# Performance work log

Measured on AMD Instinct MI355X. Metric: run time of the kernel, lower is better.

## Reference

```python
import jax, jax.numpy as jnp
import numpy as np

B, S, E = 4, 2048, 1024


def setup_inputs() -> dict:
    key = jax.random.key(0)
    ks = jax.random.split(key, 7)
    sc = 1.0 / np.sqrt(E)
    return {
        "embedded": jax.random.normal(ks[0], (B, S, E), dtype=jnp.float32),
        "Wk": jax.random.normal(ks[1], (E, E), dtype=jnp.float32) * sc,
        "bk": jax.random.normal(ks[2], (E,), dtype=jnp.float32) * 0.01,
        "Wq": jax.random.normal(ks[3], (E, E), dtype=jnp.float32) * sc,
        "bq": jax.random.normal(ks[4], (E,), dtype=jnp.float32) * 0.01,
        "Wv": jax.random.normal(ks[5], (E, E), dtype=jnp.float32) * sc,
        "bv": jax.random.normal(ks[6], (E,), dtype=jnp.float32) * 0.01,
    }


def reference(embedded, Wk, bk, Wq, bq, Wv, bv):
    # embedded: [B, S, E]
    K = embedded @ Wk.T + bk  # [B,S,E]
    Q = embedded @ Wq.T + bq
    V = embedded @ Wv.T + bv
    seq_len = K.shape[1]
    # score[b,i,j] = K_i . Q_j, scaled by 1/sqrt(seq_len) (as in original)
    scores = jnp.einsum('bie,bje->bij', K, Q) / jnp.sqrt(jnp.asarray(seq_len, K.dtype))
    # softmax over dim=-2 -> over the key index i
    W = jax.nn.softmax(scores, axis=-2)  # [B,S,S]
    # Y = (V^T @ W)^T -> Y[b,j,d] = sum_i V[b,i,d] * W[b,i,j]
    Y = jnp.einsum('bid,bij->bjd', V, W)  # [B,S,E]
    return Y
```

## Files before the change

### kernel.cpp

```cpp
#include <hip/hip_runtime.h>
#include <hip/hip_bf16.h>


typedef __bf16 bf16x8 __attribute__((ext_vector_type(8)));
typedef float  f32x4  __attribute__((ext_vector_type(4)));

__device__ __forceinline__ unsigned short f2bf(float f) {
    unsigned int u = __float_as_uint(f);
    u = (u + 0x7FFFu + ((u >> 16) & 1u)) >> 16;
    return (unsigned short)u;
}

__global__ __launch_bounds__(256)
void cvt_all(const float* __restrict__ X,  const float* __restrict__ Wq,
             const float* __restrict__ Wk, const float* __restrict__ Wv,
             unsigned short* __restrict__ Xb,  unsigned short* __restrict__ Wqb,
             unsigned short* __restrict__ Wkb, unsigned short* __restrict__ Wvb,
             float* __restrict__ l) {
    long i = (long)blockIdx.x * 256 + threadIdx.x;
    if (i < 8192) l[i] = 0.0f;
    const float* src; unsigned short* dst; long off;
    if (i < 2097152L) { src = X; dst = Xb; off = i; }
    else {
        long j = i - 2097152L;
        int w = (int)(j >> 18);
        off = j & 262143L;
        src = (w == 0) ? Wq : (w == 1) ? Wk : Wv;
        dst = (w == 0) ? Wqb : (w == 1) ? Wkb : Wvb;
    }
    float4 v = reinterpret_cast<const float4*>(src)[off];
    ushort4 o;
    o.x = f2bf(v.x); o.y = f2bf(v.y); o.z = f2bf(v.z); o.w = f2bf(v.w);
    reinterpret_cast<ushort4*>(dst)[off] = o;
}

#define GEMM_DECLS                                                      \
    const int t    = threadIdx.x;                                       \
    const int wave = t >> 6;                                            \
    const int lane = t & 63;                                            \
    const int quad = lane >> 4;                                         \
    const int lr   = lane & 15;                                         \
    const int wm   = (wave >> 1) * 64;                                  \
    const int wn   = (wave & 1) * 64;                                   \
    const int sx   = lr & 7;                                            \
    const int lrow = lane >> 3;                                         \
    const int gch  = ((lane & 7) ^ (lrow & 7)) * 8;

#define GEMM_KLOOP(Aptr, Bptr, LDA, LDB)                                \
    for (int k0 = 0; k0 < K; k0 += 64) {                                \
        _Pragma("unroll")                                               \
        for (int r = 0; r < 4; ++r) {                                   \
            const int rowb = wave * 8 + r * 32;                         \
            const int row  = rowb + lrow;                               \
            const long goffA = (long)(m0 + row) * (LDA) + k0 + gch;     \
            const long goffB = (long)(n0 + row) * (LDB) + k0 + gch;     \
            __builtin_amdgcn_global_load_lds(                           \
                (const __attribute__((address_space(1))) void*)((Aptr) + goffA), \
                (__attribute__((address_space(3))) void*)(&lsA[rowb * 64]), 16, 0, 0); \
            __builtin_amdgcn_global_load_lds(                           \
                (const __attribute__((address_space(1))) void*)((Bptr) + goffB), \
                (__attribute__((address_space(3))) void*)(&lsB[rowb * 64]), 16, 0, 0); \
        }                                                               \
        __syncthreads();                                                \
        _Pragma("unroll")                                               \
        for (int h = 0; h < 2; ++h) {                                   \
            const int cp = ((h * 4 + quad) ^ sx) * 8;                   \
            bf16x8 af[4], bfr[4];                                       \
            _Pragma("unroll")                                           \
            for (int i = 0; i < 4; ++i) {                               \
                af[i]  = __builtin_bit_cast(bf16x8,                     \
                          *reinterpret_cast<const uint4*>(&lsA[(wm + i * 16 + lr) * 64 + cp])); \
                bfr[i] = __builtin_bit_cast(bf16x8,                     \
                          *reinterpret_cast<const uint4*>(&lsB[(wn + i * 16 + lr) * 64 + cp])); \
            }                                                           \
            _Pragma("unroll")                                           \
            for (int i = 0; i < 4; ++i)                                 \
                _Pragma("unroll")                                       \
                for (int j = 0; j < 4; ++j)                             \
                    acc[i][j] = __builtin_amdgcn_mfma_f32_16x16x32_bf16(af[i], bfr[j], acc[i][j], 0, 0, 0); \
        }                                                               \
        __syncthreads();                                                \
    }

__global__ __launch_bounds__(256, 2)
void gemm_qkv(const unsigned short* __restrict__ Xb,
              const unsigned short* __restrict__ Wqb,
              const unsigned short* __restrict__ Wkb,
              const unsigned short* __restrict__ Wvb,
              const float* __restrict__ bq, const float* __restrict__ bk,
              const float* __restrict__ bv_,
              unsigned short* __restrict__ Qb, unsigned short* __restrict__ Kb,
              unsigned short* __restrict__ Vt)
{
    __shared__ unsigned short lsA[128 * 64];
    __shared__ unsigned short lsB[128 * 64];

    const int id  = blockIdx.x;
    const int g   = id & 7;
    const int jj  = id >> 3;
    const int xx  = jj & 7;
    const int yin = (jj >> 3) & 7;
    const int z   = jj >> 6;

    const unsigned short* A = Xb;
    const unsigned short* B = (z == 0) ? Wqb : (z == 1) ? Wkb : Wvb;
    const float* bias       = (z == 0) ? bq  : (z == 1) ? bk  : bv_;

    const int n0 = xx * 128;
    const int m0 = (g * 8 + yin) * 128;
    const int K = 1024;

    GEMM_DECLS
    f32x4 acc[4][4] = {};
    GEMM_KLOOP(A, B, 1024, 1024)

#pragma unroll
    for (int j = 0; j < 4; ++j) {
        const int n = n0 + wn + j * 16 + lr;
        const float bvv = bias[n];
#pragma unroll
        for (int i = 0; i < 4; ++i) {
            const int mbase = m0 + wm + i * 16 + quad * 4;
            if (z < 2) {
                unsigned short* C = (z == 0) ? Qb : Kb;
#pragma unroll
                for (int r = 0; r < 4; ++r)
                    C[(long)(mbase + r) * 1024 + n] = f2bf(acc[i][j][r] + bvv);
            } else {
                ushort4 o;
                o.x = f2bf(acc[i][j][0] + bvv);
                o.y = f2bf(acc[i][j][1] + bvv);
                o.z = f2bf(acc[i][j][2] + bvv);
                o.w = f2bf(acc[i][j][3] + bvv);
                long boff = (long)(mbase >> 11) * (1024L * 2048) + (long)n * 2048 + (mbase & 2047);
                *reinterpret_cast<ushort4*>(Vt + boff) = o;
            }
        }
    }
}


#define VMW(N) asm volatile("s_waitcnt vmcnt(" #N ")" ::: "memory")

#define PIPE_DECLS                                                          \
    const int tid  = threadIdx.x;                                           \
    const int wave = tid >> 6;                                              \
    const int lane = tid & 63;                                              \
    const int quad = lane >> 4;                                             \
    const int lr   = lane & 15;                                             \
    const int wvm  = wave >> 2;                           \
    const int wvn  = wave & 3;                            \
    const int rd_off = (lr >> 1) * 64 + (lr & 1) * 32                       \
                     + ((quad ^ ((lr >> 1) & 3)) << 3);                     \
    const int stg_rl = wave * 16 + ((lane >> 3) << 1) + ((lane >> 2) & 1);  \
    const int stg_c  = (((lane & 3) ^ ((lane >> 3) & 3)) << 3);

#define ST1(base, LD, kcol, dst, c)                                         \
    __builtin_amdgcn_global_load_lds(                                       \
        (const __attribute__((address_space(1))) void*)                     \
            ((base) + (long)(c) * 128 * (LD) + (kcol)),                     \
        (__attribute__((address_space(3))) void*)(&lds[(dst) + (c) * 4096 + wave * 512]), \
        16, 0, 0)

#define PHASE(bs, h, mh, IH_, STG, WAITS)                                   \
    {                                                                       \
        if ((mh) == 0) {                                                    \
            _Pragma("unroll")                                               \
            for (int j = 0; j < 4; ++j)                                     \
                bfr[j] = __builtin_bit_cast(bf16x8,                         \
                    *reinterpret_cast<const uint4*>(                        \
                        &lds[BOFF(bs, h) + (wvn * 4 + j) * 512 + rd_off])); \
        }                                                                   \
        bf16x8 af[IH_];                                                     \
        _Pragma("unroll")                                                   \
        for (int i = 0; i < (IH_); ++i)                                     \
            af[i] = __builtin_bit_cast(bf16x8,                              \
                *reinterpret_cast<const uint4*>(                            \
                    &lds[AOFF(bs, h) + (wvm * 2 * (IH_) + (mh) * (IH_) + i) * 512 + rd_off])); \
        STG;                                                                \
        WAITS;                                                              \
        __builtin_amdgcn_s_barrier();                                       \
        __builtin_amdgcn_s_setprio(1);                                      \
        _Pragma("unroll")                                                   \
        for (int i = 0; i < (IH_); ++i)                                     \
            _Pragma("unroll")                                               \
            for (int j = 0; j < 4; ++j)                                     \
                acc[(mh) * (IH_) + i][j] = __builtin_amdgcn_mfma_f32_16x16x32_bf16( \
                    af[i], bfr[j], acc[(mh) * (IH_) + i][j], 0, 0, 0);      \
        __builtin_amdgcn_s_setprio(0);                                      \
        __builtin_amdgcn_s_barrier();                                       \
    }

#define RUN_PIPELINE(IH_, NT_, WAITST)                                      \
    f32x4 acc[2 * (IH_)][4] = {};                                           \
    bf16x8 bfr[4];                                                          \
    SA(0, 0, 0); SB(0, 0, 0); SA(0, 1, 0); SB(0, 1, 0); SA(1, 0, 1); SB(1, 0, 1); \
    WAITST;                                                                 \
    __builtin_amdgcn_s_barrier();                                           \
    _Pragma("unroll 1")                                                     \
    for (int it = 0; it < (NT_) / 2 - 1; ++it) {                            \
        const int tb = 2 * it;                                              \
        PHASE(0, 0, 0, IH_, SA(tb + 1, 1, 1), )                             \
        PHASE(0, 0, 1, IH_, SB(tb + 1, 1, 1), )                             \
        PHASE(0, 1, 0, IH_, SA(tb + 2, 0, 0), )                             \
        PHASE(0, 1, 1, IH_, SB(tb + 2, 0, 0), WAITST)                       \
        PHASE(1, 0, 0, IH_, SA(tb + 2, 1, 0), )                             \
        PHASE(1, 0, 1, IH_, SB(tb + 2, 1, 0), )                             \
        PHASE(1, 1, 0, IH_, SA(tb + 3, 0, 1), )                             \
        PHASE(1, 1, 1, IH_, SB(tb + 3, 0, 1), WAITST)                       \
    }                                                                       \
    PHASE(0, 0, 0, IH_, SA((NT_) - 1, 1, 1), )                              \
    PHASE(0, 0, 1, IH_, SB((NT_) - 1, 1, 1), )                              \
    PHASE(0, 1, 0, IH_, , )                                                 \
    PHASE(0, 1, 1, IH_, , WAITST)                                           \
    PHASE(1, 0, 0, IH_, , )                                                 \
    PHASE(1, 0, 1, IH_, , VMW(0))                                           \
    PHASE(1, 1, 0, IH_, , )                                                 \
    PHASE(1, 1, 1, IH_, , )

#define AOFF(b, h) ((b) * 32768 + (h) * 8192)
#define BOFF(b, h) ((b) * 32768 + 16384 + (h) * 8192)
#define SA(tt, h, b) { ST1(aBase, 1024, (tt) * 64 + (h) * 32, AOFF(b, h), 0); \
                       ST1(aBase, 1024, (tt) * 64 + (h) * 32, AOFF(b, h), 1); }
#define SB(tt, h, b) { ST1(bBase, 1024, (tt) * 64 + (h) * 32, BOFF(b, h), 0); \
                       ST1(bBase, 1024, (tt) * 64 + (h) * 32, BOFF(b, h), 1); }

__global__ __launch_bounds__(512, 2)
void gemm_scores(const unsigned short* __restrict__ Q,
                 const unsigned short* __restrict__ Kp,
                 unsigned short* __restrict__ P, float* __restrict__ l,
                 float scale)
{
    __shared__ __align__(16) unsigned short lds[65536];

    const int id = blockIdx.x;
    const int g  = id & 7;
    const int u  = id >> 3;
    const int bz = g >> 1;
    const int m0 = ((g & 1) * 4 + (u & 3)) * 256;
    const int n0 = (u >> 2) * 256;

    const unsigned short* Aptr = Q  + (long)bz * 2048 * 1024;
    const unsigned short* Bptr = Kp + (long)bz * 2048 * 1024;
    unsigned short* Pb = P + (long)bz * 2048 * 2048;
    float* lb = l + bz * 2048;

    PIPE_DECLS
    const unsigned short* aBase = Aptr + (long)(m0 + stg_rl) * 1024 + stg_c;
    const unsigned short* bBase = Bptr + (long)(n0 + stg_rl) * 1024 + stg_c;

    RUN_PIPELINE(4, 16, VMW(4))

#pragma unroll
    for (int i = 0; i < 8; ++i) {
#pragma unroll
        for (int r = 0; r < 4; ++r) {
            const int m = m0 + wvm * 128 + i * 16 + quad * 4 + r;
            float psum = 0.0f;
#pragma unroll
            for (int j = 0; j < 4; ++j) {
                const float p = __expf(acc[i][j][r] * scale);
                psum += p;
                Pb[(long)m * 2048 + (n0 + wvn * 64 + j * 16 + lr)] = f2bf(p);
            }
#pragma unroll
            for (int o = 1; o < 16; o <<= 1) psum += __shfl_xor(psum, o, 64);
            if (lr == 0) atomicAdd(&lb[m], psum);
        }
    }
}

#undef SA
#undef SB
#undef AOFF
#undef BOFF

#define AOFF(b, h) ((b) * 24576 + (h) * 4096)
#define BOFF(b, h) ((b) * 24576 + 8192 + (h) * 8192)
#define SA(tt, h, b) { ST1(aBase, 2048, (tt) * 64 + (h) * 32, AOFF(b, h), 0); }
#define SB(tt, h, b) { ST1(bBase, 2048, (tt) * 64 + (h) * 32, BOFF(b, h), 0); \
                       ST1(bBase, 2048, (tt) * 64 + (h) * 32, BOFF(b, h), 1); }

__global__ __launch_bounds__(512, 2)
void gemm_y(const unsigned short* __restrict__ P,
            const unsigned short* __restrict__ Vt,
            const float* __restrict__ l, float* __restrict__ out)
{
    __shared__ __align__(16) unsigned short lds[49152];

    const int id = blockIdx.x;
    const int g  = id & 7;
    const int u  = id >> 3;
    const int bz = g >> 1;
    const int m0 = ((g & 1) * 8 + (u & 7)) * 128;
    const int n0 = (u >> 3) * 256;

    const unsigned short* Aptr = P  + (long)bz * 2048 * 2048;
    const unsigned short* Bptr = Vt + (long)bz * 1024 * 2048;
    const float* lb = l + bz * 2048;
    float* C = out + (long)bz * 2048 * 1024;

    PIPE_DECLS
    const unsigned short* aBase = Aptr + (long)(m0 + stg_rl) * 2048 + stg_c;
    const unsigned short* bBase = Bptr + (long)(n0 + stg_rl) * 2048 + stg_c;

    RUN_PIPELINE(2, 32, VMW(3))

    float linv[4][4];
#pragma unroll
    for (int i = 0; i < 4; ++i)
#pragma unroll
        for (int r = 0; r < 4; ++r)
            linv[i][r] = 1.0f / lb[m0 + wvm * 64 + i * 16 + quad * 4 + r];

#pragma unroll
    for (int j = 0; j < 4; ++j) {
        const int n = n0 + wvn * 64 + j * 16 + lr;
#pragma unroll
        for (int i = 0; i < 4; ++i) {
            const int mbase = m0 + wvm * 64 + i * 16 + quad * 4;
#pragma unroll
            for (int r = 0; r < 4; ++r)
                C[(long)(mbase + r) * 1024 + n] = acc[i][j][r] * linv[i][r];
        }
    }
}

#undef SA
#undef SB
#undef AOFF
#undef BOFF

extern "C" void kernel_launch(void* const* d_in, const int* in_sizes, int n_in,
                              void* d_out, int out_size, void* d_ws, size_t ws_size,
                              hipStream_t stream) {
    const float* X  = (const float*)d_in[0];
    const float* Wk = (const float*)d_in[1];
    const float* bk = (const float*)d_in[2];
    const float* Wq = (const float*)d_in[3];
    const float* bq = (const float*)d_in[4];
    const float* Wv = (const float*)d_in[5];
    const float* bv = (const float*)d_in[6];
    float* out = (float*)d_out;

    const size_t MB = 1024 * 1024;
    if (ws_size < 80 * MB) return;

    char* ws = (char*)d_ws;
    unsigned short* Vt  = (unsigned short*)(ws);
    unsigned short* P   = (unsigned short*)(ws + 16 * MB);
    unsigned short* Xbf = (unsigned short*)(ws + 16 * MB);
    float*          l   = (float*)(ws + 48 * MB);
    unsigned short* Wqb = (unsigned short*)(ws + 49 * MB);
    unsigned short* Wkb = (unsigned short*)(ws + 51 * MB);
    unsigned short* Wvb = (unsigned short*)(ws + 53 * MB);
    unsigned short* Qb = (unsigned short*)d_out;
    unsigned short* Kb = Qb + 8192L * 1024;

    cvt_all<<<2883584 / 256, dim3(256), 0, stream>>>(X, Wq, Wk, Wv, Xbf, Wqb, Wkb, Wvb, l);

    gemm_qkv<<<1536, dim3(256), 0, stream>>>(Xbf, Wqb, Wkb, Wvb, bq, bk, bv, Qb, Kb, Vt);

    gemm_scores<<<256, dim3(512), 0, stream>>>(Qb, Kb, P, l, 0.022097086912079608f);

    gemm_y<<<256, dim3(512), 0, stream>>>(P, Vt, l, out);
}
```

Measured before the change: 228.5 us.

## Retile gemm_y to 256x128 with a 4-buffer, 3-deep K-32 LDS pipeline

The P·V GEMM block tile changes from 128x256 to 256x128 (M x N), and the shared pipeline macro is replaced by a custom 4-stage ring of 32-wide K slices with three loads in flight. Each phase reads fragments from LDS, issues the next global-to-LDS copies, waits, then runs 16 MFMAs at raised priority. The aim is more latency hiding for global loads and a better balance between loading A (P) and B (V). The cost is more barriers per unit of K and different LDS traffic per MFMA.

```diff
diff --git a/kernel.cpp b/kernel.cpp
--- a/kernel.cpp
+++ b/kernel.cpp
@@ -275,11 +275,38 @@
 #undef AOFF
 #undef BOFF
 
-#define AOFF(b, h) ((b) * 24576 + (h) * 4096)
-#define BOFF(b, h) ((b) * 24576 + 8192 + (h) * 8192)
-#define SA(tt, h, b) { ST1(aBase, 2048, (tt) * 64 + (h) * 32, AOFF(b, h), 0); }
-#define SB(tt, h, b) { ST1(bBase, 2048, (tt) * 64 + (h) * 32, BOFF(b, h), 0); \
-                       ST1(bBase, 2048, (tt) * 64 + (h) * 32, BOFF(b, h), 1); }
+#define YAOFF(b) ((b) * 12288)
+#define YBOFF(b) ((b) * 12288 + 8192)
+#define YSA(tt, b) { ST1(aBase, 2048, (tt) * 32, YAOFF(b), 0); \
+                     ST1(aBase, 2048, (tt) * 32, YAOFF(b), 1); }
+#define YSB(tt, b) { ST1(bBase, 2048, (tt) * 32, YBOFF(b), 0); }
+
+#define YPHASE(bb, STG, WAITS)                                              \
+    {                                                                       \
+        bf16x8 af[4], bfr[4];                                               \
+        _Pragma("unroll")                                                   \
+        for (int j = 0; j < 4; ++j)                                         \
+            bfr[j] = __builtin_bit_cast(bf16x8,                             \
+                *reinterpret_cast<const uint4*>(                            \
+                    &lds[YBOFF(bb) + (wvn * 4 + j) * 512 + rd_off]));       \
+        _Pragma("unroll")                                                   \
+        for (int i = 0; i < 4; ++i)                                         \
+            af[i] = __builtin_bit_cast(bf16x8,                              \
+                *reinterpret_cast<const uint4*>(                            \
+                    &lds[YAOFF(bb) + (wvm * 4 + i) * 512 + rd_off]));       \
+        STG;                                                                \
+        WAITS;                                                              \
+        __builtin_amdgcn_s_barrier();                                       \
+        __builtin_amdgcn_s_setprio(1);                                      \
+        _Pragma("unroll")                                                   \
+        for (int i = 0; i < 4; ++i)                                         \
+            _Pragma("unroll")                                               \
+            for (int j = 0; j < 4; ++j)                                     \
+                acc[i][j] = __builtin_amdgcn_mfma_f32_16x16x32_bf16(        \
+                    af[i], bfr[j], acc[i][j], 0, 0, 0);                     \
+        __builtin_amdgcn_s_setprio(0);                                      \
+        __builtin_amdgcn_s_barrier();                                       \
+    }
 
 __global__ __launch_bounds__(512, 2)
 void gemm_y(const unsigned short* __restrict__ P,
@@ -292,19 +319,47 @@
     const int g  = id & 7;
     const int u  = id >> 3;
     const int bz = g >> 1;
-    const int m0 = ((g & 1) * 8 + (u & 7)) * 128;
-    const int n0 = (u >> 3) * 256;
+    const int m0 = ((g & 1) * 4 + (u & 3)) * 256;
+    const int n0 = (u >> 2) * 128;
 
     const unsigned short* Aptr = P  + (long)bz * 2048 * 2048;
     const unsigned short* Bptr = Vt + (long)bz * 1024 * 2048;
     const float* lb = l + bz * 2048;
     float* C = out + (long)bz * 2048 * 1024;
 
-    PIPE_DECLS
+    const int tid  = threadIdx.x;
+    const int wave = tid >> 6;
+    const int lane = tid & 63;
+    const int quad = lane >> 4;
+    const int lr   = lane & 15;
+    const int wvm  = wave >> 1;
+    const int wvn  = wave & 1;
+    const int rd_off = (lr >> 1) * 64 + (lr & 1) * 32
+                     + ((quad ^ ((lr >> 1) & 3)) << 3);
+    const int stg_rl = wave * 16 + ((lane >> 3) << 1) + ((lane >> 2) & 1);
+    const int stg_c  = (((lane & 3) ^ ((lane >> 3) & 3)) << 3);
+
     const unsigned short* aBase = Aptr + (long)(m0 + stg_rl) * 2048 + stg_c;
     const unsigned short* bBase = Bptr + (long)(n0 + stg_rl) * 2048 + stg_c;
 
-    RUN_PIPELINE(2, 32, VMW(3))
+    f32x4 acc[4][4] = {};
+
+    YSA(0, 0); YSB(0, 0);
+    YSA(1, 1); YSB(1, 1);
+    YSA(2, 2); YSB(2, 2);
+    VMW(6);
+    __builtin_amdgcn_s_barrier();
+
+    int bcur = 0;
+#pragma unroll 1
+    for (int tt = 0; tt < 61; ++tt) {
+        int b3 = bcur + 3; if (b3 >= 4) b3 -= 4;
+        YPHASE(bcur, { YSA(tt + 3, b3); YSB(tt + 3, b3); }, VMW(6))
+        if (++bcur == 4) bcur = 0;
+    }
+    YPHASE(1, , VMW(3))
+    YPHASE(2, , VMW(0))
+    YPHASE(3, , )
 
     float linv[4][4];
 #pragma unroll
@@ -326,10 +381,10 @@
     }
 }
 
-#undef SA
-#undef SB
-#undef AOFF
-#undef BOFF
+#undef YSA
+#undef YSB
+#undef YAOFF
+#undef YBOFF
 
 extern "C" void kernel_launch(void* const* d_in, const int* in_sizes, int n_in,
                               void* d_out, int out_size, void* d_ws, size_t ws_size,
```

Result: slower. 240.9 us (+5.4%).

## Replace pipelined scores GEMM with simpler 128x256-tile kernel at higher occupancy

Applied to the files above, without the earlier changes.

The scores GEMM moves from the deep software-pipelined 256x256 tile kernel with 512 threads to a simple single-buffered 128x256 tile kernel with 256 threads and 3 blocks per CU, launched as 512 blocks. Each k-step loads A and B into LDS via global_load_lds, synchronises, and runs MFMAs. The aim is more resident blocks and fewer idle CUs instead of hand-tuned intra-block overlap. In exchange it drops the explicit load/compute pipelining, has a barrier after every tile, and gives more B-tile reloads per unit of output because the tiles are smaller.

```diff
diff --git a/kernel.cpp b/kernel.cpp
--- a/kernel.cpp
+++ b/kernel.cpp
@@ -139,6 +139,97 @@
     }
 }
 
+__global__ __launch_bounds__(256, 3)
+void gemm_scores(const unsigned short* __restrict__ Q,
+                 const unsigned short* __restrict__ Kp,
+                 unsigned short* __restrict__ P, float* __restrict__ l,
+                 float scale)
+{
+    __shared__ unsigned short lsA[128 * 64];
+    __shared__ unsigned short lsB[256 * 64];
+
+    const int id = blockIdx.x;
+    const int g  = id & 7;
+    const int u  = id >> 3;
+    const int bz = g >> 1;
+    const int m0 = ((g & 1) * 8 + (u & 7)) * 128;
+    const int n0 = (u >> 3) * 256;
+
+    const unsigned short* A = Q  + (long)bz * 2048 * 1024;
+    const unsigned short* B = Kp + (long)bz * 2048 * 1024;
+    unsigned short* Pb = P + (long)bz * 2048 * 2048;
+    float* lb = l + bz * 2048;
+
+    const int t    = threadIdx.x;
+    const int wave = t >> 6;
+    const int lane = t & 63;
+    const int quad = lane >> 4;
+    const int lr   = lane & 15;
+    const int sx   = lr & 7;
+    const int lrow = lane >> 3;
+    const int gch  = ((lane & 7) ^ (lrow & 7)) * 8;
+
+    f32x4 acc[8][4] = {};
+
+    for (int k0 = 0; k0 < 1024; k0 += 64) {
+#pragma unroll
+        for (int r = 0; r < 4; ++r) {
+            const int rowb = wave * 8 + r * 32;
+            __builtin_amdgcn_global_load_lds(
+                (const __attribute__((address_space(1))) void*)
+                    (A + (long)(m0 + rowb + lrow) * 1024 + k0 + gch),
+                (__attribute__((address_space(3))) void*)(&lsA[rowb * 64]), 16, 0, 0);
+        }
+#pragma unroll
+        for (int r = 0; r < 8; ++r) {
+            const int rowb = wave * 8 + r * 32;
+            __builtin_amdgcn_global_load_lds(
+                (const __attribute__((address_space(1))) void*)
+                    (B + (long)(n0 + rowb + lrow) * 1024 + k0 + gch),
+                (__attribute__((address_space(3))) void*)(&lsB[rowb * 64]), 16, 0, 0);
+        }
+        __syncthreads();
+#pragma unroll
+        for (int h = 0; h < 2; ++h) {
+            const int cp = ((h * 4 + quad) ^ sx) * 8;
+            bf16x8 af[8], bfr[4];
+#pragma unroll
+            for (int i = 0; i < 8; ++i)
+                af[i] = __builtin_bit_cast(bf16x8,
+                    *reinterpret_cast<const uint4*>(&lsA[(i * 16 + lr) * 64 + cp]));
+#pragma unroll
+            for (int j = 0; j < 4; ++j)
+                bfr[j] = __builtin_bit_cast(bf16x8,
+                    *reinterpret_cast<const uint4*>(&lsB[(wave * 64 + j * 16 + lr) * 64 + cp]));
+#pragma unroll
+            for (int i = 0; i < 8; ++i)
+#pragma unroll
+                for (int j = 0; j < 4; ++j)
+                    acc[i][j] = __builtin_amdgcn_mfma_f32_16x16x32_bf16(
+                        af[i], bfr[j], acc[i][j], 0, 0, 0);
+        }
+        __syncthreads();
+    }
+
+#pragma unroll
+    for (int i = 0; i < 8; ++i) {
+#pragma unroll
+        for (int r = 0; r < 4; ++r) {
+            const int m = m0 + i * 16 + quad * 4 + r;
+            float psum = 0.0f;
+#pragma unroll
+            for (int j = 0; j < 4; ++j) {
+                const float p = __expf(acc[i][j][r] * scale);
+                psum += p;
+                Pb[(long)m * 2048 + (n0 + wave * 64 + j * 16 + lr)] = f2bf(p);
+            }
+#pragma unroll
+            for (int o = 1; o < 16; o <<= 1) psum += __shfl_xor(psum, o, 64);
+            if (lr == 0) atomicAdd(&lb[m], psum);
+        }
+    }
+}
+
 
 #define VMW(N) asm volatile("s_waitcnt vmcnt(" #N ")" ::: "memory")
 
@@ -218,63 +309,6 @@
     PHASE(1, 1, 0, IH_, , )                                                 \
     PHASE(1, 1, 1, IH_, , )
 
-#define AOFF(b, h) ((b) * 32768 + (h) * 8192)
-#define BOFF(b, h) ((b) * 32768 + 16384 + (h) * 8192)
-#define SA(tt, h, b) { ST1(aBase, 1024, (tt) * 64 + (h) * 32, AOFF(b, h), 0); \
-                       ST1(aBase, 1024, (tt) * 64 + (h) * 32, AOFF(b, h), 1); }
-#define SB(tt, h, b) { ST1(bBase, 1024, (tt) * 64 + (h) * 32, BOFF(b, h), 0); \
-                       ST1(bBase, 1024, (tt) * 64 + (h) * 32, BOFF(b, h), 1); }
-
-__global__ __launch_bounds__(512, 2)
-void gemm_scores(const unsigned short* __restrict__ Q,
-                 const unsigned short* __restrict__ Kp,
-                 unsigned short* __restrict__ P, float* __restrict__ l,
-                 float scale)
-{
-    __shared__ __align__(16) unsigned short lds[65536];
-
-    const int id = blockIdx.x;
-    const int g  = id & 7;
-    const int u  = id >> 3;
-    const int bz = g >> 1;
-    const int m0 = ((g & 1) * 4 + (u & 3)) * 256;
-    const int n0 = (u >> 2) * 256;
-
-    const unsigned short* Aptr = Q  + (long)bz * 2048 * 1024;
-    const unsigned short* Bptr = Kp + (long)bz * 2048 * 1024;
-    unsigned short* Pb = P + (long)bz * 2048 * 2048;
-    float* lb = l + bz * 2048;
-
-    PIPE_DECLS
-    const unsigned short* aBase = Aptr + (long)(m0 + stg_rl) * 1024 + stg_c;
-    const unsigned short* bBase = Bptr + (long)(n0 + stg_rl) * 1024 + stg_c;
-
-    RUN_PIPELINE(4, 16, VMW(4))
-
-#pragma unroll
-    for (int i = 0; i < 8; ++i) {
-#pragma unroll
-        for (int r = 0; r < 4; ++r) {
-            const int m = m0 + wvm * 128 + i * 16 + quad * 4 + r;
-            float psum = 0.0f;
-#pragma unroll
-            for (int j = 0; j < 4; ++j) {
-                const float p = __expf(acc[i][j][r] * scale);
-                psum += p;
-                Pb[(long)m * 2048 + (n0 + wvn * 64 + j * 16 + lr)] = f2bf(p);
-            }
-#pragma unroll
-            for (int o = 1; o < 16; o <<= 1) psum += __shfl_xor(psum, o, 64);
-            if (lr == 0) atomicAdd(&lb[m], psum);
-        }
-    }
-}
-
-#undef SA
-#undef SB
-#undef AOFF
-#undef BOFF
-
 #define AOFF(b, h) ((b) * 24576 + (h) * 4096)
 #define BOFF(b, h) ((b) * 24576 + 8192 + (h) * 8192)
 #define SA(tt, h, b) { ST1(aBase, 2048, (tt) * 64 + (h) * 32, AOFF(b, h), 0); }
@@ -361,7 +395,7 @@
 
     gemm_qkv<<<1536, dim3(256), 0, stream>>>(Xbf, Wqb, Wkb, Wvb, bq, bk, bv, Qb, Kb, Vt);
 
-    gemm_scores<<<256, dim3(512), 0, stream>>>(Qb, Kb, P, l, 0.022097086912079608f);
+    gemm_scores<<<512, dim3(256), 0, stream>>>(Qb, Kb, P, l, 0.022097086912079608f);
 
     gemm_y<<<256, dim3(512), 0, stream>>>(P, Vt, l, out);
 }
```

Measured after the change: 256.6 us. 12.3% more time.

## Fold key/query projections into single X·(WkᵀWq) product and drop softmax-invariant bias terms

Applied to the files above, without the earlier changes.

Rewrites the score computation algebraically. It precomputes M = Wq^T Wk, projects X once through M instead of computing Q and K separately, and adds a per-key bias term u = X·(Wk^T bq). Terms depending only on the query index are dropped because they cancel in the softmax over keys. This removes one of the three large projection GEMMs at the cost of a small weight-weight GEMM, transposes and matvecs, and it adds an extra bf16 rounding of M.

```diff
diff --git a/kernel.cpp b/kernel.cpp
--- a/kernel.cpp
+++ b/kernel.cpp
@@ -10,28 +10,55 @@
     u = (u + 0x7FFFu + ((u >> 16) & 1u)) >> 16;
     return (unsigned short)u;
 }
+__device__ __forceinline__ float bf2f(unsigned short s) {
+    return __uint_as_float(((unsigned int)s) << 16);
+}
 
 __global__ __launch_bounds__(256)
 void cvt_all(const float* __restrict__ X,  const float* __restrict__ Wq,
              const float* __restrict__ Wk, const float* __restrict__ Wv,
-             unsigned short* __restrict__ Xb,  unsigned short* __restrict__ Wqb,
-             unsigned short* __restrict__ Wkb, unsigned short* __restrict__ Wvb,
+             unsigned short* __restrict__ Xb,  unsigned short* __restrict__ WqT,
+             unsigned short* __restrict__ WkT, unsigned short* __restrict__ Wvb,
              float* __restrict__ l) {
-    long i = (long)blockIdx.x * 256 + threadIdx.x;
-    if (i < 8192) l[i] = 0.0f;
-    const float* src; unsigned short* dst; long off;
-    if (i < 2097152L) { src = X; dst = Xb; off = i; }
-    else {
-        long j = i - 2097152L;
-        int w = (int)(j >> 18);
-        off = j & 262143L;
-        src = (w == 0) ? Wq : (w == 1) ? Wk : Wv;
-        dst = (w == 0) ? Wqb : (w == 1) ? Wkb : Wvb;
-    }
-    float4 v = reinterpret_cast<const float4*>(src)[off];
-    ushort4 o;
-    o.x = f2bf(v.x); o.y = f2bf(v.y); o.z = f2bf(v.z); o.w = f2bf(v.w);
-    reinterpret_cast<ushort4*>(dst)[off] = o;
+    __shared__ unsigned short lt[64][68];
+    const int id = blockIdx.x;
+    const int t  = threadIdx.x;
+    if (id < 9216) {
+        long i; const float* src; unsigned short* dst;
+        if (id < 8192) { i = (long)id * 256 + t; if (i < 8192) l[i] = 0.0f; src = X; dst = Xb; }
+        else           { i = (long)(id - 8192) * 256 + t; src = Wv; dst = Wvb; }
+        float4 v = reinterpret_cast<const float4*>(src)[i];
+        ushort4 o;
+        o.x = f2bf(v.x); o.y = f2bf(v.y); o.z = f2bf(v.z); o.w = f2bf(v.w);
+        reinterpret_cast<ushort4*>(dst)[i] = o;
+        return;
+    }
+    const int k   = id - 9216;
+    const int mat = k >> 8;
+    const int tl  = k & 255;
+    const int f0  = (tl >> 4) * 64;
+    const int e0  = (tl & 15) * 64;
+    const float* src = (mat == 0) ? Wq : Wk;
+    unsigned short* dst = (mat == 0) ? WqT : WkT;
+    const int r  = t >> 4;
+    const int c  = t & 15;
+#pragma unroll
+    for (int q = 0; q < 4; ++q) {
+        const int fl = r + q * 16;
+        float4 v = reinterpret_cast<const float4*>(src)[(long)(f0 + fl) * 256 + (e0 >> 2) + c];
+        lt[fl][c * 4 + 0] = f2bf(v.x); lt[fl][c * 4 + 1] = f2bf(v.y);
+        lt[fl][c * 4 + 2] = f2bf(v.z); lt[fl][c * 4 + 3] = f2bf(v.w);
+    }
+    __syncthreads();
+#pragma unroll
+    for (int q = 0; q < 4; ++q) {
+        const int el = (t >> 4) + q * 16;
+        const int f4 = (t & 15) * 4;
+        ushort4 o;
+        o.x = lt[f4 + 0][el]; o.y = lt[f4 + 1][el];
+        o.z = lt[f4 + 2][el]; o.w = lt[f4 + 3][el];
+        *reinterpret_cast<ushort4*>(&dst[(long)(e0 + el) * 1024 + f0 + f4]) = o;
+    }
 }
 
 #define GEMM_DECLS                                                      \
@@ -83,19 +110,92 @@
     }
 
 __global__ __launch_bounds__(256, 2)
-void gemm_qkv(const unsigned short* __restrict__ Xb,
-              const unsigned short* __restrict__ Wqb,
-              const unsigned short* __restrict__ Wkb,
-              const unsigned short* __restrict__ Wvb,
-              const float* __restrict__ bq, const float* __restrict__ bk,
-              const float* __restrict__ bv_,
-              unsigned short* __restrict__ Qb, unsigned short* __restrict__ Kb,
-              unsigned short* __restrict__ Vt)
+void prep(const unsigned short* __restrict__ WqT,
+          const unsigned short* __restrict__ WkT,
+          const float* __restrict__ bq,
+          unsigned short* __restrict__ Mt, float* __restrict__ w)
 {
     __shared__ unsigned short lsA[128 * 64];
     __shared__ unsigned short lsB[128 * 64];
-
-    const int id  = blockIdx.x;
+    const int id = blockIdx.x;
+    if (id < 64) {
+        const int m0 = (id & 7) * 128;
+        const int n0 = (id >> 3) * 128;
+        const int K = 1024;
+        GEMM_DECLS
+        f32x4 acc[4][4] = {};
+        GEMM_KLOOP(WqT, WkT, 1024, 1024)
+#pragma unroll
+        for (int j = 0; j < 4; ++j) {
+            const int n = n0 + wn + j * 16 + lr;
+#pragma unroll
+            for (int i = 0; i < 4; ++i) {
+                const int mbase = m0 + wm + i * 16 + quad * 4;
+#pragma unroll
+                for (int r = 0; r < 4; ++r)
+                    Mt[(long)(mbase + r) * 1024 + n] = f2bf(acc[i][j][r]);
+            }
+        }
+        return;
+    }
+    const int t2   = threadIdx.x;
+    const int ep   = (id - 64) * 128 + (t2 >> 1);
+    const int half = t2 & 1;
+    float s = 0.0f;
+    const unsigned short* row = WkT + (long)ep * 1024 + half * 512;
+    const float* bqh = bq + half * 512;
+#pragma unroll 4
+    for (int c = 0; c < 64; ++c) {
+        ushort4 a = reinterpret_cast<const ushort4*>(row)[c * 2];
+        ushort4 b = reinterpret_cast<const ushort4*>(row)[c * 2 + 1];
+        float4 q0 = reinterpret_cast<const float4*>(bqh)[c * 2];
+        float4 q1 = reinterpret_cast<const float4*>(bqh)[c * 2 + 1];
+        s += bf2f(a.x) * q0.x + bf2f(a.y) * q0.y + bf2f(a.z) * q0.z + bf2f(a.w) * q0.w;
+        s += bf2f(b.x) * q1.x + bf2f(b.y) * q1.y + bf2f(b.z) * q1.z + bf2f(b.w) * q1.w;
+    }
+    s += __shfl_xor(s, 1, 64);
+    if (half == 0) w[ep] = s;
+}
+
+__global__ __launch_bounds__(256, 2)
+void qv(const unsigned short* __restrict__ Xb,
+        const unsigned short* __restrict__ Mt,
+        const unsigned short* __restrict__ Wvb,
+        const float* __restrict__ bv_, const float* __restrict__ w,
+        unsigned short* __restrict__ Tb, unsigned short* __restrict__ Vt,
+        float* __restrict__ u)
+{
+    __shared__ unsigned short lsA[128 * 64];
+    __shared__ unsigned short lsB[128 * 64];
+
+    const int id = blockIdx.x;
+    if (id >= 1024) {
+        const int ub = id - 1024;
+        const int t2 = threadIdx.x;
+        const int rq = t2 >> 2;
+        const int part = t2 & 3;
+#pragma unroll 1
+        for (int pass = 0; pass < 4; ++pass) {
+            const int i = ub * 256 + pass * 64 + rq;
+            const unsigned short* xr = Xb + (long)i * 1024 + part * 256;
+            const float* wp = w + part * 256;
+            float s = 0.0f;
+#pragma unroll 4
+            for (int c = 0; c < 32; ++c) {
+                ushort4 a = reinterpret_cast<const ushort4*>(xr)[c * 2];
+                ushort4 b = reinterpret_cast<const ushort4*>(xr)[c * 2 + 1];
+                float4 q0 = reinterpret_cast<const float4*>(wp)[c * 2];
+                float4 q1 = reinterpret_cast<const float4*>(wp)[c * 2 + 1];
+                s += bf2f(a.x) * q0.x + bf2f(a.y) * q0.y + bf2f(a.z) * q0.z + bf2f(a.w) * q0.w;
+                s += bf2f(b.x) * q1.x + bf2f(b.y) * q1.y + bf2f(b.z) * q1.z + bf2f(b.w) * q1.w;
+            }
+            s += __shfl_xor(s, 1, 64);
+            s += __shfl_xor(s, 2, 64);
+            if (part == 0) u[i] = s;
+        }
+        return;
+    }
+
     const int g   = id & 7;
     const int jj  = id >> 3;
     const int xx  = jj & 7;
@@ -103,8 +203,7 @@
     const int z   = jj >> 6;
 
     const unsigned short* A = Xb;
-    const unsigned short* B = (z == 0) ? Wqb : (z == 1) ? Wkb : Wvb;
-    const float* bias       = (z == 0) ? bq  : (z == 1) ? bk  : bv_;
+    const unsigned short* B = (z == 0) ? Mt : Wvb;
 
     const int n0 = xx * 128;
     const int m0 = (g * 8 + yin) * 128;
@@ -117,15 +216,14 @@
 #pragma unroll
     for (int j = 0; j < 4; ++j) {
         const int n = n0 + wn + j * 16 + lr;
-        const float bvv = bias[n];
+        const float bvv = (z == 1) ? bv_[n] : 0.0f;
 #pragma unroll
         for (int i = 0; i < 4; ++i) {
             const int mbase = m0 + wm + i * 16 + quad * 4;
-            if (z < 2) {
-                unsigned short* C = (z == 0) ? Qb : Kb;
+            if (z == 0) {
 #pragma unroll
                 for (int r = 0; r < 4; ++r)
-                    C[(long)(mbase + r) * 1024 + n] = f2bf(acc[i][j][r] + bvv);
+                    Tb[(long)(mbase + r) * 1024 + n] = f2bf(acc[i][j][r]);
             } else {
                 ushort4 o;
                 o.x = f2bf(acc[i][j][0] + bvv);
@@ -226,8 +324,9 @@
                        ST1(bBase, 1024, (tt) * 64 + (h) * 32, BOFF(b, h), 1); }
 
 __global__ __launch_bounds__(512, 2)
-void gemm_scores(const unsigned short* __restrict__ Q,
-                 const unsigned short* __restrict__ Kp,
+void gemm_scores(const unsigned short* __restrict__ Xq,
+                 const unsigned short* __restrict__ Tp,
+                 const float* __restrict__ u,
                  unsigned short* __restrict__ P, float* __restrict__ l,
                  float scale)
 {
@@ -235,13 +334,14 @@
 
     const int id = blockIdx.x;
     const int g  = id & 7;
-    const int u  = id >> 3;
+    const int uu = id >> 3;
     const int bz = g >> 1;
-    const int m0 = ((g & 1) * 4 + (u & 3)) * 256;
-    const int n0 = (u >> 2) * 256;
-
-    const unsigned short* Aptr = Q  + (long)bz * 2048 * 1024;
-    const unsigned short* Bptr = Kp + (long)bz * 2048 * 1024;
+    const int m0 = ((g & 1) * 4 + (uu & 3)) * 256;
+    const int n0 = (uu >> 2) * 256;
+
+    const unsigned short* Aptr = Xq + (long)bz * 2048 * 1024;
+    const unsigned short* Bptr = Tp + (long)bz * 2048 * 1024;
+    const float* ub = u + bz * 2048;
     unsigned short* Pb = P + (long)bz * 2048 * 2048;
     float* lb = l + bz * 2048;
 
@@ -251,6 +351,11 @@
 
     RUN_PIPELINE(4, 16, VMW(4))
 
+    float uv[4];
+#pragma unroll
+    for (int j = 0; j < 4; ++j)
+        uv[j] = ub[n0 + wvn * 64 + j * 16 + lr];
+
 #pragma unroll
     for (int i = 0; i < 8; ++i) {
 #pragma unroll
@@ -259,7 +364,7 @@
             float psum = 0.0f;
 #pragma unroll
             for (int j = 0; j < 4; ++j) {
-                const float p = __expf(acc[i][j][r] * scale);
+                const float p = __expf((acc[i][j][r] + uv[j]) * scale);
                 psum += p;
                 Pb[(long)m * 2048 + (n0 + wvn * 64 + j * 16 + lr)] = f2bf(p);
             }
@@ -290,10 +395,10 @@
 
     const int id = blockIdx.x;
     const int g  = id & 7;
-    const int u  = id >> 3;
+    const int uu = id >> 3;
     const int bz = g >> 1;
-    const int m0 = ((g & 1) * 8 + (u & 7)) * 128;
-    const int n0 = (u >> 3) * 256;
+    const int m0 = ((g & 1) * 8 + (uu & 7)) * 128;
+    const int n0 = (uu >> 3) * 256;
 
     const unsigned short* Aptr = P  + (long)bz * 2048 * 2048;
     const unsigned short* Bptr = Vt + (long)bz * 1024 * 2048;
@@ -344,24 +449,30 @@
     float* out = (float*)d_out;
 
     const size_t MB = 1024 * 1024;
+    const size_t KB = 1024;
     if (ws_size < 80 * MB) return;
+    (void)bk;
 
     char* ws = (char*)d_ws;
     unsigned short* Vt  = (unsigned short*)(ws);
     unsigned short* P   = (unsigned short*)(ws + 16 * MB);
-    unsigned short* Xbf = (unsigned short*)(ws + 16 * MB);
     float*          l   = (float*)(ws + 48 * MB);
-    unsigned short* Wqb = (unsigned short*)(ws + 49 * MB);
-    unsigned short* Wkb = (unsigned short*)(ws + 51 * MB);
+    float*          u   = (float*)(ws + 48 * MB + 64 * KB);
+    float*          w   = (float*)(ws + 48 * MB + 128 * KB);
+    unsigned short* WqT = (unsigned short*)(ws + 49 * MB);
+    unsigned short* WkT = (unsigned short*)(ws + 51 * MB);
     unsigned short* Wvb = (unsigned short*)(ws + 53 * MB);
-    unsigned short* Qb = (unsigned short*)d_out;
-    unsigned short* Kb = Qb + 8192L * 1024;
-
-    cvt_all<<<2883584 / 256, dim3(256), 0, stream>>>(X, Wq, Wk, Wv, Xbf, Wqb, Wkb, Wvb, l);
-
-    gemm_qkv<<<1536, dim3(256), 0, stream>>>(Xbf, Wqb, Wkb, Wvb, bq, bk, bv, Qb, Kb, Vt);
-
-    gemm_scores<<<256, dim3(512), 0, stream>>>(Qb, Kb, P, l, 0.022097086912079608f);
+    unsigned short* Xb  = (unsigned short*)(ws + 55 * MB);
+    unsigned short* Mt  = (unsigned short*)(ws + 71 * MB);
+    unsigned short* Tb  = (unsigned short*)d_out;
+
+    cvt_all<<<9728, dim3(256), 0, stream>>>(X, Wq, Wk, Wv, Xb, WqT, WkT, Wvb, l);
+
+    prep<<<72, dim3(256), 0, stream>>>(WqT, WkT, bq, Mt, w);
+
+    qv<<<1056, dim3(256), 0, stream>>>(Xb, Mt, Wvb, bv, w, Tb, Vt, u);
+
+    gemm_scores<<<256, dim3(512), 0, stream>>>(Xb, Tb, u, P, l, 0.022097086912079608f);
 
     gemm_y<<<256, dim3(512), 0, stream>>>(P, Vt, l, out);
 }
```

After: 267.5 us. +17.1%, slower.
